# Optimization experiments

Measured on AMD Instinct MI355X. Metric: run time of the kernel, lower is better.

## Reference

```python
import jax, jax.numpy as jnp
import numpy as np
import math

SEQ, BATCH, HID, HEADS = 2048, 2, 2048, 16
HEAD_DIM = HID // HEADS
ROPE_BASE = 10000.0


def setup_inputs() -> dict:
    key = jax.random.key(0)
    k1, k2, k3 = jax.random.split(key, 3)
    hidden_states = jax.random.normal(k1, (SEQ, BATCH, HID), dtype=jnp.float32)
    # causal mask: True means masked (gpt2-style attention_mask_func fills with -10000)
    attention_mask = jnp.triu(jnp.ones((SEQ, SEQ), dtype=bool), k=1)[None, None, :, :]
    w_qkv = jax.random.normal(k2, (3 * HID, HID), dtype=jnp.float32) * 0.02
    b_qkv = jnp.zeros((3 * HID,), dtype=jnp.float32)
    w_dense = jax.random.normal(k3, (HID, HID), dtype=jnp.float32) * 0.02
    b_dense = jnp.zeros((HID,), dtype=jnp.float32)
    return {"hidden_states": hidden_states, "attention_mask": attention_mask,
            "w_qkv": w_qkv, "b_qkv": b_qkv, "w_dense": w_dense, "b_dense": b_dense}


def _rotary_cos_sin(seq_len, dim, dtype):
    inv_freq = 1.0 / (ROPE_BASE ** (jnp.arange(0, dim, 2, dtype=jnp.float32) / dim))
    t = jnp.arange(seq_len, dtype=jnp.float32)
    freqs = jnp.einsum("s,d->sd", t, inv_freq)
    emb = jnp.concatenate([freqs, freqs], axis=-1)  # [s, dim]
    # broadcast to [s, 1, 1, dim] over (batch, heads)
    return jnp.cos(emb)[:, None, None, :].astype(dtype), jnp.sin(emb)[:, None, None, :].astype(dtype)


def _rotate_half(x):
    x1, x2 = jnp.split(x, 2, axis=-1)
    return jnp.concatenate([-x2, x1], axis=-1)


def reference(hidden_states, attention_mask, w_qkv, b_qkv, w_dense, b_dense):
    s, b, h = hidden_states.shape
    # QKV projection: [s, b, 3h] -> [s, b, nh, 3*hd] -> split
    mixed = hidden_states @ w_qkv.T + b_qkv
    mixed = mixed.reshape(s, b, HEADS, 3 * HEAD_DIM)
    q, k, v = jnp.split(mixed, 3, axis=-1)  # each [s, b, nh, hd]
    # rotary (rotary_pct == 1 -> full head dim)
    cos, sin = _rotary_cos_sin(s, HEAD_DIM, q.dtype)
    q = q * cos + _rotate_half(q) * sin
    k = k * cos + _rotate_half(k) * sin
    # attention scores [b, nh, s_q, s_k]
    norm_factor = math.sqrt(HEAD_DIM)
    scores = jnp.einsum("sbhd,tbhd->bhst", q, k) / norm_factor
    scores = jnp.where(attention_mask, jnp.asarray(-10000.0, scores.dtype), scores)
    # softmax in fp32
    probs = jax.nn.softmax(scores.astype(jnp.float32), axis=-1).astype(scores.dtype)
    # context [s, b, nh, hd] -> [s, b, h]
    context = jnp.einsum("bhst,tbhd->sbhd", probs, v).reshape(s, b, h)
    # dense with skip_bias_add: bias returned separately
    output = context @ w_dense.T
    return output, b_dense
```

## Files before the change

kernel.cpp:

```cpp
#include <hip/hip_runtime.h>
#include <cstdint>
#include <math.h>


typedef unsigned short u16;
typedef __bf16 bf16x8 __attribute__((ext_vector_type(8)));
typedef float floatx4 __attribute__((ext_vector_type(4)));

#define SEQ 2048
#define BATCH 2
#define HID 2048
#define NH 16
#define HD 128
#define LDA 72

__device__ __forceinline__ u16 f2bf(float f) {
  union { float f; uint32_t u; } v; v.f = f;
  uint32_t u = v.u;
  return (u16)((u + 0x7FFFu + ((u >> 16) & 1u)) >> 16);
}

__device__ __forceinline__ void st8_bf16(u16* dst, const float* s) {
  uint32_t pk[4];
#pragma unroll
  for (int j = 0; j < 4; j++)
    pk[j] = (uint32_t)f2bf(s[2 * j]) | ((uint32_t)f2bf(s[2 * j + 1]) << 16);
  *(uint4*)dst = make_uint4(pk[0], pk[1], pk[2], pk[3]);
}

__device__ __forceinline__ void gl16(const u16* g, u16* l) {
  __builtin_amdgcn_global_load_lds(
      (const __attribute__((address_space(1))) void*)g,
      (__attribute__((address_space(3))) void*)l, 16, 0, 0);
}

__global__ __launch_bounds__(256) void cvt_inputs(
    const float* __restrict__ W, const float* __restrict__ Hid,
    u16* __restrict__ wb, u16* __restrict__ Ah) {
  const int blk = blockIdx.x;
  const int c0 = threadIdx.x * 8;
  const float* src;
  u16* dst;
  if (blk < 4096) {
    int dt = blk >> 7, r = blk & 127;
    int srow = (dt < 16) ? ((dt * 3 + 1) * 128 + r) : (((dt - 16) * 3) * 128 + r);
    src = W + (size_t)srow * HID;
    dst = wb + (size_t)blk * HID;
  } else {
    int r = blk - 4096;
    src = Hid + (size_t)r * HID;
    dst = Ah + (size_t)r * HID;
  }
  float t[8];
  *(floatx4*)&t[0] = *(const floatx4*)(src + c0);
  *(floatx4*)&t[4] = *(const floatx4*)(src + c0 + 4);
  st8_bf16(dst + c0, t);
}

__global__ __launch_bounds__(256) void cvt_wd(const float* __restrict__ W,
                                              u16* __restrict__ wd) {
  const int r = blockIdx.x;
  const int c0 = threadIdx.x * 8;
  float t[8];
  const float* src = W + (size_t)r * HID;
  *(floatx4*)&t[0] = *(const floatx4*)(src + c0);
  *(floatx4*)&t[4] = *(const floatx4*)(src + c0 + 4);
  st8_bf16(wd + (size_t)r * HID + c0, t);
}

__global__ __launch_bounds__(256, 2) void qkv_qk(
    const u16* __restrict__ Ah, const u16* __restrict__ wb,
    const float* __restrict__ bias, u16* __restrict__ Qw,
    u16* __restrict__ Kw) {
  __shared__ __align__(16) u16 As[128 * 64];
  __shared__ __align__(16) u16 Bs[128 * 64];
  const int tid = threadIdx.x;
  const int wv = tid >> 6, lane = tid & 63;
  const int quad = lane >> 4, l16 = lane & 15;
  const int wt = blockIdx.x;
  const int bm = blockIdx.y;
  const int rowA0 = bm * 128;
  const int wm = (wv >> 1) * 64;
  const int wn = (wv & 1) * 32;
  const int ntoff[4] = {wn, wn + 16, wn + 64, wn + 80};

  const int lrow = wv * 32 + (lane >> 3);
  const int lcol = (lane & 7) * 8;
  const u16* Ag = Ah + (size_t)(rowA0 + lrow) * HID + lcol;
  const u16* Bg = wb + ((size_t)wt * 128 + lrow) * HID + lcol;
  u16* Al = &As[(wv * 32) * 64];
  u16* Bl = &Bs[(wv * 32) * 64];

  floatx4 acc[4][4];
#pragma unroll
  for (int i = 0; i < 4; i++)
#pragma unroll
    for (int j = 0; j < 4; j++) acc[i][j] = (floatx4){0.f, 0.f, 0.f, 0.f};

  for (int kb = 0; kb < HID; kb += 64) {
#pragma unroll
    for (int j = 0; j < 4; j++) {
      gl16(Ag + (size_t)j * 8 * HID + kb, Al + j * 8 * 64);
      gl16(Bg + (size_t)j * 8 * HID + kb, Bl + j * 8 * 64);
    }
    __syncthreads();
#pragma unroll
    for (int ks = 0; ks < 64; ks += 32) {
      bf16x8 af[4], bfr[4];
#pragma unroll
      for (int mi = 0; mi < 4; mi++)
        af[mi] = *(const bf16x8*)&As[(wm + mi * 16 + l16) * 64 + ks + quad * 8];
#pragma unroll
      for (int ni = 0; ni < 4; ni++)
        bfr[ni] = *(const bf16x8*)&Bs[(ntoff[ni] + l16) * 64 + ks + quad * 8];
#pragma unroll
      for (int mi = 0; mi < 4; mi++)
#pragma unroll
        for (int ni = 0; ni < 4; ni++)
          acc[mi][ni] = __builtin_amdgcn_mfma_f32_16x16x32_bf16(
              af[mi], bfr[ni], acc[mi][ni], 0, 0, 0);
    }
    __syncthreads();
  }

  const int seg = (wt < 16) ? 1 : 0;
  const int head = wt & 15;
  u16* dst = seg ? Kw : Qw;
  float bv[4];
#pragma unroll
  for (int ni = 0; ni < 4; ni++)
    bv[ni] = bias[(head * 3 + seg) * 128 + ntoff[ni] + l16];
  const float RC = 0.20762050593045951f;
  const float f0 = exp2f(-(float)(wn + l16) * RC);
  const float f1 = exp2f(-(float)(wn + 16 + l16) * RC);

#pragma unroll
  for (int mi = 0; mi < 4; mi++) {
#pragma unroll
    for (int reg = 0; reg < 4; reg++) {
      int r = rowA0 + wm + mi * 16 + quad * 4 + reg;
      int s = r >> 1, b = r & 1;
      size_t base = ((size_t)(b * NH + head) * SEQ + s) * HD;
      float sv, cv;
      sincosf((float)s * f0, &sv, &cv);
      {
        float lo = acc[mi][0][reg] + bv[0];
        float hi = acc[mi][2][reg] + bv[2];
        dst[base + wn + l16] = f2bf(lo * cv - hi * sv);
        dst[base + wn + l16 + 64] = f2bf(hi * cv + lo * sv);
      }
      sincosf((float)s * f1, &sv, &cv);
      {
        float lo = acc[mi][1][reg] + bv[1];
        float hi = acc[mi][3][reg] + bv[3];
        dst[base + wn + 16 + l16] = f2bf(lo * cv - hi * sv);
        dst[base + wn + 16 + l16 + 64] = f2bf(hi * cv + lo * sv);
      }
    }
  }
}

__global__ __launch_bounds__(256, 2) void qkv_v(
    const u16* __restrict__ Ah, const float* __restrict__ W,
    const float* __restrict__ bias, u16* __restrict__ Vt) {
  __shared__ __align__(16) u16 As[128 * 64];
  __shared__ __align__(16) u16 Bs[128 * LDA];
  const int tid = threadIdx.x;
  const int wv = tid >> 6, lane = tid & 63;
  const int quad = lane >> 4, l16 = lane & 15;
  const int head = blockIdx.x;
  const int bm = blockIdx.y;
  const int rowA0 = bm * 128;
  const int rowB0 = (head * 3 + 2) * 128;
  const int wm = (wv >> 1) * 64;
  const int wn = (wv & 1) * 32;
  const int ntoff[4] = {wn, wn + 16, wn + 64, wn + 80};

  const int lrow = wv * 32 + (lane >> 3);
  const int lcol = (lane & 7) * 8;
  const u16* Ag = Ah + (size_t)(rowA0 + lrow) * HID + lcol;
  u16* Al = &As[(wv * 32) * 64];

  floatx4 acc[4][4];
#pragma unroll
  for (int i = 0; i < 4; i++)
#pragma unroll
    for (int j = 0; j < 4; j++) acc[i][j] = (floatx4){0.f, 0.f, 0.f, 0.f};

  for (int kb = 0; kb < HID; kb += 64) {
    float fb[4][8];
#pragma unroll
    for (int i = 0; i < 4; i++) {
      int c = i * 256 + tid;
      int row = c >> 3, k8 = (c & 7) * 8;
      const float* sb = &W[(size_t)(rowB0 + row) * HID + kb + k8];
      *(floatx4*)&fb[i][0] = *(const floatx4*)sb;
      *(floatx4*)&fb[i][4] = *(const floatx4*)(sb + 4);
    }
    __syncthreads();
#pragma unroll
    for (int j = 0; j < 4; j++)
      gl16(Ag + (size_t)j * 8 * HID + kb, Al + j * 8 * 64);
#pragma unroll
    for (int i = 0; i < 4; i++) {
      int c = i * 256 + tid;
      int row = c >> 3, k8 = (c & 7) * 8;
      st8_bf16(&Bs[row * LDA + k8], fb[i]);
    }
    __syncthreads();
#pragma unroll
    for (int ks = 0; ks < 64; ks += 32) {
      bf16x8 af[4], bfr[4];
#pragma unroll
      for (int mi = 0; mi < 4; mi++)
        af[mi] = *(const bf16x8*)&As[(wm + mi * 16 + l16) * 64 + ks + quad * 8];
#pragma unroll
      for (int ni = 0; ni < 4; ni++)
        bfr[ni] = *(const bf16x8*)&Bs[(ntoff[ni] + l16) * LDA + ks + quad * 8];
#pragma unroll
      for (int mi = 0; mi < 4; mi++)
#pragma unroll
        for (int ni = 0; ni < 4; ni++)
          acc[mi][ni] = __builtin_amdgcn_mfma_f32_16x16x32_bf16(
              af[mi], bfr[ni], acc[mi][ni], 0, 0, 0);
    }
  }
  __syncthreads();

  float bv[4];
#pragma unroll
  for (int ni = 0; ni < 4; ni++)
    bv[ni] = bias[(head * 3 + 2) * 128 + ntoff[ni] + l16];
#pragma unroll
  for (int mi = 0; mi < 4; mi++) {
#pragma unroll
    for (int ni = 0; ni < 4; ni++) {
      int d = ntoff[ni] + l16;
#pragma unroll
      for (int reg = 0; reg < 4; reg++) {
        int r = rowA0 + wm + mi * 16 + quad * 4 + reg;
        int s = r >> 1, b = r & 1;
        Vt[((size_t)(b * NH + head) * HD + d) * SEQ + s] =
            f2bf(acc[mi][ni][reg] + bv[ni]);
      }
    }
  }
}

__global__ __launch_bounds__(256, 2) void attn(
    const u16* __restrict__ Qw, const u16* __restrict__ Kw,
    const u16* __restrict__ Vt, u16* __restrict__ ctx) {
  __shared__ __align__(16) u16 Ks[64 * 128];
  __shared__ __align__(16) u16 Vs[128 * 64];
  __shared__ __align__(16) u16 Pl[4 * 32 * 72];

  const int tid = threadIdx.x;
  const int wv = tid >> 6, lane = tid & 63;
  const int quad = lane >> 4, l16 = lane & 15;
  const int bh = blockIdx.y;
  const int b = bh >> 4, h = bh & 15;
  const int qt = (bh < 16) ? blockIdx.x : 15 - blockIdx.x;
  const int sw = qt * 128 + wv * 32;
  const size_t bhoff = (size_t)bh * SEQ * HD;

  bf16x8 qf[2][4];
#pragma unroll
  for (int mi = 0; mi < 2; mi++)
#pragma unroll
    for (int kc = 0; kc < 4; kc++)
      qf[mi][kc] = *(const bf16x8*)&Qw[bhoff +
                                       (size_t)(sw + mi * 16 + l16) * HD +
                                       kc * 32 + quad * 8];

  floatx4 o[2][8];
#pragma unroll
  for (int mi = 0; mi < 2; mi++)
#pragma unroll
    for (int ni = 0; ni < 8; ni++) o[mi][ni] = (floatx4){0.f, 0.f, 0.f, 0.f};
  float mst[2][4], lst[2][4];
#pragma unroll
  for (int mi = 0; mi < 2; mi++)
#pragma unroll
    for (int r = 0; r < 4; r++) { mst[mi][r] = -1e30f; lst[mi][r] = 0.f; }

  const int nt = qt * 2 + 2;
  const float SCL2 = 0.088388347648318447f * 1.442695040888963f;
  const float MSK2 = -10000.0f * 1.442695040888963f;

  for (int t = 0; t < nt; t++) {
    __syncthreads();
#pragma unroll
    for (int i = 0; i < 4; i++) {
      int c = i * 256 + tid;
      int rk = c >> 4, uk = c & 15;
      gl16(&Kw[bhoff + (size_t)(t * 64 + rk) * HD + (uk ^ (rk & 7)) * 8],
           &Ks[(i * 256 + wv * 64) * 8]);
      int rv = c >> 3, uv = c & 7;
      gl16(&Vt[bhoff + (size_t)rv * SEQ + t * 64 + (uv ^ (rv & 7)) * 8],
           &Vs[(i * 256 + wv * 64) * 8]);
    }
    __syncthreads();

    const bool active = (t * 64 <= sw + 31);
    if (active) {
      floatx4 sa[2][4];
#pragma unroll
      for (int mi = 0; mi < 2; mi++)
#pragma unroll
        for (int ni = 0; ni < 4; ni++) sa[mi][ni] = (floatx4){0.f, 0.f, 0.f, 0.f};
      __builtin_amdgcn_s_setprio(1);
#pragma unroll
      for (int kc = 0; kc < 4; kc++) {
        bf16x8 kf[4];
#pragma unroll
        for (int ni = 0; ni < 4; ni++)
          kf[ni] = *(const bf16x8*)&Ks[(ni * 16 + l16) * 128 +
                                       (((kc * 4 + quad) ^ (l16 & 7)) * 8)];
#pragma unroll
        for (int mi = 0; mi < 2; mi++)
#pragma unroll
          for (int ni = 0; ni < 4; ni++)
            sa[mi][ni] = __builtin_amdgcn_mfma_f32_16x16x32_bf16(
                qf[mi][kc], kf[ni], sa[mi][ni], 0, 0, 0);
      }
      __builtin_amdgcn_s_setprio(0);

      float alpha[2][4];
#pragma unroll
      for (int mi = 0; mi < 2; mi++) {
#pragma unroll
        for (int reg = 0; reg < 4; reg++) {
          int sq = sw + mi * 16 + quad * 4 + reg;
          float rv[4];
#pragma unroll
          for (int ni = 0; ni < 4; ni++) {
            int sk = t * 64 + ni * 16 + l16;
            float v = sa[mi][ni][reg] * SCL2;
            if (sk > sq) v = MSK2;
            rv[ni] = v;
          }
          float rmax = fmaxf(fmaxf(rv[0], rv[1]), fmaxf(rv[2], rv[3]));
          rmax = fmaxf(rmax, __shfl_xor(rmax, 1));
          rmax = fmaxf(rmax, __shfl_xor(rmax, 2));
          rmax = fmaxf(rmax, __shfl_xor(rmax, 4));
          rmax = fmaxf(rmax, __shfl_xor(rmax, 8));
          float mn = fmaxf(mst[mi][reg], rmax);
          float al = exp2f(mst[mi][reg] - mn);
          float rs = 0.f;
#pragma unroll
          for (int ni = 0; ni < 4; ni++) {
            float p = exp2f(rv[ni] - mn);
            rs += p;
            Pl[wv * 2304 + (mi * 16 + quad * 4 + reg) * 72 + ni * 16 + l16] =
                f2bf(p);
          }
          rs += __shfl_xor(rs, 1);
          rs += __shfl_xor(rs, 2);
          rs += __shfl_xor(rs, 4);
          rs += __shfl_xor(rs, 8);
          lst[mi][reg] = lst[mi][reg] * al + rs;
          mst[mi][reg] = mn;
          alpha[mi][reg] = al;
        }
      }
#pragma unroll
      for (int mi = 0; mi < 2; mi++)
#pragma unroll
        for (int ni = 0; ni < 8; ni++)
#pragma unroll
          for (int reg = 0; reg < 4; reg++)
            o[mi][ni][reg] *= alpha[mi][reg];

      __builtin_amdgcn_s_setprio(1);
#pragma unroll
      for (int kc = 0; kc < 2; kc++) {
        bf16x8 pf[2];
#pragma unroll
        for (int mi = 0; mi < 2; mi++)
          pf[mi] = *(const bf16x8*)&Pl[wv * 2304 + (mi * 16 + l16) * 72 +
                                       kc * 32 + quad * 8];
#pragma unroll
        for (int ni = 0; ni < 8; ni++) {
          bf16x8 vf = *(const bf16x8*)&Vs[(ni * 16 + l16) * 64 +
                                          (((kc * 4 + quad) ^ (l16 & 7)) * 8)];
#pragma unroll
          for (int mi = 0; mi < 2; mi++)
            o[mi][ni] = __builtin_amdgcn_mfma_f32_16x16x32_bf16(
                pf[mi], vf, o[mi][ni], 0, 0, 0);
        }
      }
      __builtin_amdgcn_s_setprio(0);
    }
  }

#pragma unroll
  for (int mi = 0; mi < 2; mi++) {
#pragma unroll
    for (int reg = 0; reg < 4; reg++) {
      float inv = 1.0f / lst[mi][reg];
      int sq = sw + mi * 16 + quad * 4 + reg;
      size_t rbase = ((size_t)(sq * BATCH + b)) * HID + h * HD;
#pragma unroll
      for (int ni = 0; ni < 8; ni++)
        ctx[rbase + ni * 16 + l16] = f2bf(o[mi][ni][reg] * inv);
    }
  }
}

__global__ __launch_bounds__(256, 2) void dense_gemm(
    const u16* __restrict__ A, const u16* __restrict__ Wd,
    float* __restrict__ out) {
  __shared__ __align__(16) u16 As[128 * 64];
  __shared__ __align__(16) u16 Bs[128 * 64];
  const int tid = threadIdx.x;
  const int wv = tid >> 6, lane = tid & 63;
  const int quad = lane >> 4, l16 = lane & 15;
  const int bn = blockIdx.x, bm = blockIdx.y;
  const int rowA0 = bm * 128, rowB0 = bn * 128;
  const int wm = (wv >> 1) * 64;
  const int wn = (wv & 1) * 64;
  const int ntoff[4] = {wn, wn + 16, wn + 32, wn + 48};

  const int lrow = wv * 32 + (lane >> 3);
  const int lcol = (lane & 7) * 8;
  const u16* Ag = A + (size_t)(rowA0 + lrow) * HID + lcol;
  const u16* Bg = Wd + (size_t)(rowB0 + lrow) * HID + lcol;
  u16* Al = &As[(wv * 32) * 64];
  u16* Bl = &Bs[(wv * 32) * 64];

  floatx4 acc[4][4];
#pragma unroll
  for (int i = 0; i < 4; i++)
#pragma unroll
    for (int j = 0; j < 4; j++) acc[i][j] = (floatx4){0.f, 0.f, 0.f, 0.f};

  for (int kb = 0; kb < HID; kb += 64) {
#pragma unroll
    for (int j = 0; j < 4; j++) {
      gl16(Ag + (size_t)j * 8 * HID + kb, Al + j * 8 * 64);
      gl16(Bg + (size_t)j * 8 * HID + kb, Bl + j * 8 * 64);
    }
    __syncthreads();
#pragma unroll
    for (int ks = 0; ks < 64; ks += 32) {
      bf16x8 af[4], bfr[4];
#pragma unroll
      for (int mi = 0; mi < 4; mi++)
        af[mi] = *(const bf16x8*)&As[(wm + mi * 16 + l16) * 64 + ks + quad * 8];
#pragma unroll
      for (int ni = 0; ni < 4; ni++)
        bfr[ni] = *(const bf16x8*)&Bs[(ntoff[ni] + l16) * 64 + ks + quad * 8];
#pragma unroll
      for (int mi = 0; mi < 4; mi++)
#pragma unroll
        for (int ni = 0; ni < 4; ni++)
          acc[mi][ni] = __builtin_amdgcn_mfma_f32_16x16x32_bf16(
              af[mi], bfr[ni], acc[mi][ni], 0, 0, 0);
    }
    __syncthreads();
  }

#pragma unroll
  for (int mi = 0; mi < 4; mi++)
#pragma unroll
    for (int reg = 0; reg < 4; reg++) {
      int r = rowA0 + wm + mi * 16 + quad * 4 + reg;
#pragma unroll
      for (int ni = 0; ni < 4; ni++)
        out[(size_t)r * HID + bn * 128 + ntoff[ni] + l16] = acc[mi][ni][reg];
    }
}

__global__ void copy_bias(const float* __restrict__ bd, float* __restrict__ out) {
  int i = blockIdx.x * 256 + threadIdx.x;
  if (i < HID) out[(size_t)SEQ * BATCH * HID + i] = bd[i];
}

extern "C" void kernel_launch(void* const* d_in, const int* in_sizes, int n_in,
                              void* d_out, int out_size, void* d_ws,
                              size_t ws_size, hipStream_t stream) {
  const float *hidden = nullptr, *w_qkv = nullptr, *b_qkv = nullptr;
  const float *w_dense = nullptr, *b_dense = nullptr;
  for (int i = 0; i < n_in; i++) {
    long s = in_sizes[i];
    if (s == 8388608L) hidden = (const float*)d_in[i];
    else if (s == 12582912L) w_qkv = (const float*)d_in[i];
    else if (s == 6144L) b_qkv = (const float*)d_in[i];
    else if (s == 4194304L) w_dense = (const float*)d_in[i];
    else if (s == 2048L) b_dense = (const float*)d_in[i];
  }
  float* out = (float*)d_out;

  char* ws = (char*)d_ws;
  u16* Qw = (u16*)(ws);
  u16* Kw = (u16*)(ws + 16777216ll);
  u16* Vt = (u16*)(ws + 33554432ll);
  u16* wb = (u16*)(ws + 33554432ll);
  u16* Ah = (u16*)(ws + 50331648ll);
  u16* ctx = (u16*)(ws + 50331648ll);
  u16* wd = (u16*)(ws);

  cvt_inputs<<<dim3(8192), dim3(256), 0, stream>>>(w_qkv, hidden, wb, Ah);
  qkv_qk<<<dim3(32, 32), dim3(256), 0, stream>>>(Ah, wb, b_qkv, Qw, Kw);
  qkv_v<<<dim3(16, 32), dim3(256), 0, stream>>>(Ah, w_qkv, b_qkv, Vt);
  attn<<<dim3(16, 32), dim3(256), 0, stream>>>(Qw, Kw, Vt, ctx);
  cvt_wd<<<dim3(2048), dim3(256), 0, stream>>>(w_dense, wd);
  dense_gemm<<<dim3(16, 32), dim3(256), 0, stream>>>(ctx, wd, out);
  copy_bias<<<dim3(8), dim3(256), 0, stream>>>(b_dense, out);
}
```

Measured before the change: 460.0 us.

## Pre-convert V weights, double-buffer attention K/V tiles, add lazy softmax rescale

The V-projection weights are converted to bf16 in the input conversion kernel, using the output buffer as scratch, so qkv_v can fetch them with direct global-to-LDS loads instead of converting fp32 per tile. The attention kernel double-buffers K/V tiles so the next tile loads while the current one is computed. It also skips causal masking on off-diagonal tiles and skips rescaling the output accumulator unless the running max grows by more than a threshold. The P buffer changes from padded rows to an XOR swizzle. Doubling the K/V buffers raises LDS use, which may limit occupancy, and the lazy rescale lets exponent values grow up to 2^8 before renormalising.

```diff
diff --git a/kernel.cpp b/kernel.cpp
--- a/kernel.cpp
+++ b/kernel.cpp
@@ -12,7 +12,6 @@
 #define HID 2048
 #define NH 16
 #define HD 128
-#define LDA 72
 
 __device__ __forceinline__ u16 f2bf(float f) {
   union { float f; uint32_t u; } v; v.f = f;
@@ -36,7 +35,7 @@
 
 __global__ __launch_bounds__(256) void cvt_inputs(
     const float* __restrict__ W, const float* __restrict__ Hid,
-    u16* __restrict__ wb, u16* __restrict__ Ah) {
+    u16* __restrict__ wb, u16* __restrict__ Ah, u16* __restrict__ wvw) {
   const int blk = blockIdx.x;
   const int c0 = threadIdx.x * 8;
   const float* src;
@@ -46,10 +45,15 @@
     int srow = (dt < 16) ? ((dt * 3 + 1) * 128 + r) : (((dt - 16) * 3) * 128 + r);
     src = W + (size_t)srow * HID;
     dst = wb + (size_t)blk * HID;
-  } else {
+  } else if (blk < 8192) {
     int r = blk - 4096;
     src = Hid + (size_t)r * HID;
     dst = Ah + (size_t)r * HID;
+  } else {
+    int v = blk - 8192;
+    int h = v >> 7, r = v & 127;
+    src = W + (size_t)((h * 3 + 2) * 128 + r) * HID;
+    dst = wvw + (size_t)v * HID;
   }
   float t[8];
   *(floatx4*)&t[0] = *(const floatx4*)(src + c0);
@@ -161,17 +165,16 @@
 }
 
 __global__ __launch_bounds__(256, 2) void qkv_v(
-    const u16* __restrict__ Ah, const float* __restrict__ W,
+    const u16* __restrict__ Ah, const u16* __restrict__ wvw,
     const float* __restrict__ bias, u16* __restrict__ Vt) {
   __shared__ __align__(16) u16 As[128 * 64];
-  __shared__ __align__(16) u16 Bs[128 * LDA];
+  __shared__ __align__(16) u16 Bs[128 * 64];
   const int tid = threadIdx.x;
   const int wv = tid >> 6, lane = tid & 63;
   const int quad = lane >> 4, l16 = lane & 15;
   const int head = blockIdx.x;
   const int bm = blockIdx.y;
   const int rowA0 = bm * 128;
-  const int rowB0 = (head * 3 + 2) * 128;
   const int wm = (wv >> 1) * 64;
   const int wn = (wv & 1) * 32;
   const int ntoff[4] = {wn, wn + 16, wn + 64, wn + 80};
@@ -179,7 +182,9 @@
   const int lrow = wv * 32 + (lane >> 3);
   const int lcol = (lane & 7) * 8;
   const u16* Ag = Ah + (size_t)(rowA0 + lrow) * HID + lcol;
+  const u16* Bg = wvw + ((size_t)head * 128 + lrow) * HID + lcol;
   u16* Al = &As[(wv * 32) * 64];
+  u16* Bl = &Bs[(wv * 32) * 64];
 
   floatx4 acc[4][4];
 #pragma unroll
@@ -188,24 +193,10 @@
     for (int j = 0; j < 4; j++) acc[i][j] = (floatx4){0.f, 0.f, 0.f, 0.f};
 
   for (int kb = 0; kb < HID; kb += 64) {
-    float fb[4][8];
-#pragma unroll
-    for (int i = 0; i < 4; i++) {
-      int c = i * 256 + tid;
-      int row = c >> 3, k8 = (c & 7) * 8;
-      const float* sb = &W[(size_t)(rowB0 + row) * HID + kb + k8];
-      *(floatx4*)&fb[i][0] = *(const floatx4*)sb;
-      *(floatx4*)&fb[i][4] = *(const floatx4*)(sb + 4);
-    }
-    __syncthreads();
-#pragma unroll
-    for (int j = 0; j < 4; j++)
+#pragma unroll
+    for (int j = 0; j < 4; j++) {
       gl16(Ag + (size_t)j * 8 * HID + kb, Al + j * 8 * 64);
-#pragma unroll
-    for (int i = 0; i < 4; i++) {
-      int c = i * 256 + tid;
-      int row = c >> 3, k8 = (c & 7) * 8;
-      st8_bf16(&Bs[row * LDA + k8], fb[i]);
+      gl16(Bg + (size_t)j * 8 * HID + kb, Bl + j * 8 * 64);
     }
     __syncthreads();
 #pragma unroll
@@ -216,7 +207,7 @@
         af[mi] = *(const bf16x8*)&As[(wm + mi * 16 + l16) * 64 + ks + quad * 8];
 #pragma unroll
       for (int ni = 0; ni < 4; ni++)
-        bfr[ni] = *(const bf16x8*)&Bs[(ntoff[ni] + l16) * LDA + ks + quad * 8];
+        bfr[ni] = *(const bf16x8*)&Bs[(ntoff[ni] + l16) * 64 + ks + quad * 8];
 #pragma unroll
       for (int mi = 0; mi < 4; mi++)
 #pragma unroll
@@ -224,8 +215,8 @@
           acc[mi][ni] = __builtin_amdgcn_mfma_f32_16x16x32_bf16(
               af[mi], bfr[ni], acc[mi][ni], 0, 0, 0);
     }
-  }
-  __syncthreads();
+    __syncthreads();
+  }
 
   float bv[4];
 #pragma unroll
@@ -250,9 +241,9 @@
 __global__ __launch_bounds__(256, 2) void attn(
     const u16* __restrict__ Qw, const u16* __restrict__ Kw,
     const u16* __restrict__ Vt, u16* __restrict__ ctx) {
-  __shared__ __align__(16) u16 Ks[64 * 128];
-  __shared__ __align__(16) u16 Vs[128 * 64];
-  __shared__ __align__(16) u16 Pl[4 * 32 * 72];
+  __shared__ __align__(16) u16 Ks[2][64 * 128];
+  __shared__ __align__(16) u16 Vs[2][128 * 64];
+  __shared__ __align__(16) u16 Pl[4][32 * 64];
 
   const int tid = threadIdx.x;
   const int wv = tid >> 6, lane = tid & 63;
@@ -286,23 +277,31 @@
   const int nt = qt * 2 + 2;
   const float SCL2 = 0.088388347648318447f * 1.442695040888963f;
   const float MSK2 = -10000.0f * 1.442695040888963f;
+  const float THR = 8.0f;
+
+#define STAGE(bb, tt)                                                          \
+  {                                                                            \
+    _Pragma("unroll") for (int i = 0; i < 4; i++) {                            \
+      int c = i * 256 + tid;                                                   \
+      int rk = c >> 4, uk = c & 15;                                            \
+      gl16(&Kw[bhoff + (size_t)((tt) * 64 + rk) * HD + (uk ^ (rk & 7)) * 8],   \
+           &Ks[bb][(i * 256 + wv * 64) * 8]);                                  \
+      int rv_ = c >> 3, uv = c & 7;                                            \
+      gl16(&Vt[bhoff + (size_t)rv_ * SEQ + (tt) * 64 + (uv ^ (rv_ & 7)) * 8],  \
+           &Vs[bb][(i * 256 + wv * 64) * 8]);                                  \
+    }                                                                          \
+  }
+
+  STAGE(0, 0);
+  __syncthreads();
 
   for (int t = 0; t < nt; t++) {
-    __syncthreads();
-#pragma unroll
-    for (int i = 0; i < 4; i++) {
-      int c = i * 256 + tid;
-      int rk = c >> 4, uk = c & 15;
-      gl16(&Kw[bhoff + (size_t)(t * 64 + rk) * HD + (uk ^ (rk & 7)) * 8],
-           &Ks[(i * 256 + wv * 64) * 8]);
-      int rv = c >> 3, uv = c & 7;
-      gl16(&Vt[bhoff + (size_t)rv * SEQ + t * 64 + (uv ^ (rv & 7)) * 8],
-           &Vs[(i * 256 + wv * 64) * 8]);
-    }
-    __syncthreads();
+    const int cur = t & 1;
+    if (t + 1 < nt) STAGE(cur ^ 1, t + 1);
 
     const bool active = (t * 64 <= sw + 31);
     if (active) {
+      const bool diag = (t * 64 + 63 > sw);
       floatx4 sa[2][4];
 #pragma unroll
       for (int mi = 0; mi < 2; mi++)
@@ -314,8 +313,8 @@
         bf16x8 kf[4];
 #pragma unroll
         for (int ni = 0; ni < 4; ni++)
-          kf[ni] = *(const bf16x8*)&Ks[(ni * 16 + l16) * 128 +
-                                       (((kc * 4 + quad) ^ (l16 & 7)) * 8)];
+          kf[ni] = *(const bf16x8*)&Ks[cur][(ni * 16 + l16) * 128 +
+                                            (((kc * 4 + quad) ^ (l16 & 7)) * 8)];
 #pragma unroll
         for (int mi = 0; mi < 2; mi++)
 #pragma unroll
@@ -326,50 +325,65 @@
       __builtin_amdgcn_s_setprio(0);
 
       float alpha[2][4];
+      int anyr = 0;
 #pragma unroll
       for (int mi = 0; mi < 2; mi++) {
 #pragma unroll
         for (int reg = 0; reg < 4; reg++) {
-          int sq = sw + mi * 16 + quad * 4 + reg;
+          const int rr = mi * 16 + quad * 4 + reg;
+          const int sq = sw + rr;
           float rv[4];
-#pragma unroll
-          for (int ni = 0; ni < 4; ni++) {
-            int sk = t * 64 + ni * 16 + l16;
-            float v = sa[mi][ni][reg] * SCL2;
-            if (sk > sq) v = MSK2;
-            rv[ni] = v;
+          if (diag) {
+#pragma unroll
+            for (int ni = 0; ni < 4; ni++) {
+              int sk = t * 64 + ni * 16 + l16;
+              float v = sa[mi][ni][reg] * SCL2;
+              if (sk > sq) v = MSK2;
+              rv[ni] = v;
+            }
+          } else {
+#pragma unroll
+            for (int ni = 0; ni < 4; ni++) rv[ni] = sa[mi][ni][reg] * SCL2;
           }
           float rmax = fmaxf(fmaxf(rv[0], rv[1]), fmaxf(rv[2], rv[3]));
           rmax = fmaxf(rmax, __shfl_xor(rmax, 1));
           rmax = fmaxf(rmax, __shfl_xor(rmax, 2));
           rmax = fmaxf(rmax, __shfl_xor(rmax, 4));
           rmax = fmaxf(rmax, __shfl_xor(rmax, 8));
-          float mn = fmaxf(mst[mi][reg], rmax);
-          float al = exp2f(mst[mi][reg] - mn);
+          float al;
+          if (__all(rmax <= mst[mi][reg] + THR)) {
+            al = 1.0f;
+          } else {
+            float mn = fmaxf(mst[mi][reg], rmax);
+            al = exp2f(mst[mi][reg] - mn);
+            mst[mi][reg] = mn;
+            anyr = 1;
+          }
+          const float m0 = mst[mi][reg];
           float rs = 0.f;
 #pragma unroll
           for (int ni = 0; ni < 4; ni++) {
-            float p = exp2f(rv[ni] - mn);
+            float p = exp2f(rv[ni] - m0);
             rs += p;
-            Pl[wv * 2304 + (mi * 16 + quad * 4 + reg) * 72 + ni * 16 + l16] =
-                f2bf(p);
+            Pl[wv][rr * 64 + ((ni * 16 + l16) ^ ((rr & 7) << 3))] = f2bf(p);
           }
           rs += __shfl_xor(rs, 1);
           rs += __shfl_xor(rs, 2);
           rs += __shfl_xor(rs, 4);
           rs += __shfl_xor(rs, 8);
           lst[mi][reg] = lst[mi][reg] * al + rs;
-          mst[mi][reg] = mn;
           alpha[mi][reg] = al;
         }
       }
-#pragma unroll
-      for (int mi = 0; mi < 2; mi++)
-#pragma unroll
-        for (int ni = 0; ni < 8; ni++)
-#pragma unroll
-          for (int reg = 0; reg < 4; reg++)
-            o[mi][ni][reg] *= alpha[mi][reg];
+      if (anyr) {
+#pragma unroll
+        for (int mi = 0; mi < 2; mi++)
+#pragma unroll
+          for (int ni = 0; ni < 8; ni++)
+#pragma unroll
+            for (int reg = 0; reg < 4; reg++)
+              o[mi][ni][reg] *= alpha[mi][reg];
+      }
 
       __builtin_amdgcn_s_setprio(1);
 #pragma unroll
@@ -377,12 +391,14 @@
         bf16x8 pf[2];
 #pragma unroll
         for (int mi = 0; mi < 2; mi++)
-          pf[mi] = *(const bf16x8*)&Pl[wv * 2304 + (mi * 16 + l16) * 72 +
-                                       kc * 32 + quad * 8];
+          pf[mi] = *(const bf16x8*)&Pl[wv][(mi * 16 + l16) * 64 +
+                                           ((kc * 32 + quad * 8) ^
+                                            ((l16 & 7) << 3))];
 #pragma unroll
         for (int ni = 0; ni < 8; ni++) {
-          bf16x8 vf = *(const bf16x8*)&Vs[(ni * 16 + l16) * 64 +
-                                          (((kc * 4 + quad) ^ (l16 & 7)) * 8)];
+          bf16x8 vf = *(const bf16x8*)&Vs[cur][(ni * 16 + l16) * 64 +
+                                               (((kc * 4 + quad) ^ (l16 & 7)) *
+                                                8)];
 #pragma unroll
           for (int mi = 0; mi < 2; mi++)
             o[mi][ni] = __builtin_amdgcn_mfma_f32_16x16x32_bf16(
@@ -391,6 +407,7 @@
       }
       __builtin_amdgcn_s_setprio(0);
     }
+    __syncthreads();
   }
 
 #pragma unroll
@@ -405,6 +422,7 @@
         ctx[rbase + ni * 16 + l16] = f2bf(o[mi][ni][reg] * inv);
     }
   }
+#undef STAGE
 }
 
 __global__ __launch_bounds__(256, 2) void dense_gemm(
@@ -499,10 +517,11 @@
   u16* Ah = (u16*)(ws + 50331648ll);
   u16* ctx = (u16*)(ws + 50331648ll);
   u16* wd = (u16*)(ws);
-
-  cvt_inputs<<<dim3(8192), dim3(256), 0, stream>>>(w_qkv, hidden, wb, Ah);
+  u16* wvw = (u16*)d_out;
+
+  cvt_inputs<<<dim3(10240), dim3(256), 0, stream>>>(w_qkv, hidden, wb, Ah, wvw);
   qkv_qk<<<dim3(32, 32), dim3(256), 0, stream>>>(Ah, wb, b_qkv, Qw, Kw);
-  qkv_v<<<dim3(16, 32), dim3(256), 0, stream>>>(Ah, w_qkv, b_qkv, Vt);
+  qkv_v<<<dim3(16, 32), dim3(256), 0, stream>>>(Ah, wvw, b_qkv, Vt);
   attn<<<dim3(16, 32), dim3(256), 0, stream>>>(Qw, Kw, Vt, ctx);
   cvt_wd<<<dim3(2048), dim3(256), 0, stream>>>(w_dense, wd);
   dense_gemm<<<dim3(16, 32), dim3(256), 0, stream>>>(ctx, wd, out);
```

After: 474.5 us. 1.03x slower.
